# Kernel optimization log

Hardware: AMD Instinct MI355X
Metric: run time of the kernel (lower is better)

The kernel has to match this reference:

```python
import jax, jax.numpy as jnp
import numpy as np

NUM_TRAIN_PTS = 128
KNN = 32
KNN_CLEAN = 4
SIGMA = 0.01
FEAT_DIM = 128
B, N, M = 2, 40000, 40000


def knn_gather(query, pts, k):
    """Brute-force KNN. query [B,Q,3], pts [B,P,3] -> neighbors [B,Q,k,3]."""
    # squared euclidean distances [B,Q,P]
    d2 = (jnp.sum(query * query, -1, keepdims=True)
          - 2.0 * jnp.einsum('bqd,bpd->bqp', query, pts)
          + jnp.sum(pts * pts, -1)[:, None, :])
    _, idx = jax.lax.top_k(-d2, k)                # [B,Q,k]
    nn = jax.vmap(lambda p, i: p[i])(pts, idx)    # gather -> [B,Q,k,3]
    return nn


def setup_inputs() -> dict:
    key = jax.random.key(0)
    k0, k1, k2, k3, k4, k5 = jax.random.split(key, 6)
    noisy_pc = jax.random.uniform(k0, (B, N, 3), dtype=jnp.float32)
    clean_pc = jax.random.uniform(k1, (B, M, 3), dtype=jnp.float32)
    sampled_idx = jax.random.randint(k2, (NUM_TRAIN_PTS,), 0, N)
    Wf = jax.random.normal(k3, (3, FEAT_DIM), dtype=jnp.float32) * 0.1
    Wx = jax.random.normal(k4, (3, 3), dtype=jnp.float32) * 0.1
    Wc = jax.random.normal(k5, (FEAT_DIM, 3), dtype=jnp.float32) * 0.1
    return {'noisy_pc': noisy_pc, 'clean_pc': clean_pc, 'sampled_idx': sampled_idx,
            'Wf': Wf, 'Wx': Wx, 'Wc': Wc}


def reference(noisy_pc, clean_pc, sampled_idx, Wf, Wx, Wc):
    P, K, Kc = NUM_TRAIN_PTS, KNN, KNN_CLEAN
    # per-point feature extraction (stand-in for FeatureExtraction), then sample
    noisy_feat = jnp.einsum('bnd,df->bnf', noisy_pc, Wf)[:, sampled_idx, :]  # [B,P,F]
    q = noisy_pc[:, sampled_idx, :]                                          # [B,P,3]
    # first KNN: neighbors of sampled points within the noisy cloud
    f = knn_gather(q, noisy_pc, K)                                           # [B,P,K,3]
    # score network (stand-in): local offsets + conditioning feature
    estim_score = (jnp.einsum('bpkd,de->bpke', f - q[:, :, None, :], Wx)
                   + jnp.einsum('bpf,fe->bpe', noisy_feat, Wc)[:, :, None, :])  # [B,P,K,3]
    # second KNN: each neighbor point vs the clean cloud (clean shared per batch,
    # avoiding the torch .repeat of clean_pc per training point)
    knn_clean = knn_gather(f.reshape(f.shape[0], P * K, 3), clean_pc, Kc)
    knn_clean = knn_clean.reshape(f.shape[0], P, K, Kc, 3)                   # [B,P,K,Kc,3]
    ground_score = -jnp.mean(f[:, :, :, None, :] - knn_clean, axis=3)        # [B,P,K,3]
    loss = 0.5 * jnp.mean(jnp.sum((estim_score - ground_score) ** 2 * (1.0 / SIGMA), axis=-1))
    return loss
```

## Files before the change

### kernel.cpp

```cpp
#include <hip/hip_runtime.h>
#include <hip/hip_bf16.h>

#define N_PTS   40000
#define N_B     2
#define N_P     128
#define N_K     32
#define N_KC    4
#define N_FEAT  128
#define NQ2     (N_B * N_P * N_K)
#define BIGF    3.0e38f

#define K1SUB   8
#define K1RANGE (N_PTS / K1SUB)
#define QCAP1   512
#define LBUF1   320

#define QCAP    96

#define TAU2    4.0e-3f
#define TAU1    1.6e-2f

#define NG      15
#define NCELL   (NG * NG * NG)
#define GB_BLK  20
#define GB_PER  (N_PTS / GB_BLK)

#define NLOSSB  2048

__device__ int    g_sidx[N_P];
__device__ int    g_fidx[NQ2];
__device__ int    g_q1cnt[256];
__device__ unsigned long long g_q1list[256 * QCAP1];
__device__ int    g_bincnt[N_B * NCELL];
__device__ int    g_binstart[N_B * (NCELL + 1)];
__device__ int    g_cursor[N_B * NCELL];
__device__ float4 g_cpts[N_B * N_PTS];
__device__ int    g_cpidx[N_B * N_PTS];
__device__ float  g_lploss[NLOSSB];
__device__ float  g_M3[9];
__device__ float  g_WxS[9];

__device__ __forceinline__ int clampi(int v, int lo, int hi) { return v < lo ? lo : (v > hi ? hi : v); }

__device__ __forceinline__ unsigned long long packkey(float d, int idx)
{
    unsigned int u = __float_as_uint(d);
    u ^= (u >> 31) ? 0xFFFFFFFFu : 0x80000000u;
    return ((unsigned long long)u << 32) | (unsigned int)idx;
}

__device__ __forceinline__ int cell_of(float x, float y, float z)
{
    const int cx = clampi((int)(x * NG), 0, NG - 1);
    const int cy = clampi((int)(y * NG), 0, NG - 1);
    const int cz = clampi((int)(z * NG), 0, NG - 1);
    return cx + NG * (cy + NG * cz);
}

__global__ __launch_bounds__(256) void setup_kernel(
    const float* __restrict__ clean,
    const void*  __restrict__ sidx_raw,
    const float* __restrict__ Wf,
    const float* __restrict__ Wx,
    const float* __restrict__ Wc)
{
    __shared__ int hist[NCELL];
    __shared__ int flags[4];
    const int blk = blockIdx.x;
    const int tid = threadIdx.x;

    if (blk < N_B * GB_BLK) {
        const int bb = blk / GB_BLK;
        const int sb = blk % GB_BLK;
        const float* cb = clean + bb * (N_PTS * 3);

        for (int i = tid; i < NCELL; i += 256) hist[i] = 0;
        __syncthreads();

        const int j0 = sb * GB_PER;
        for (int j = j0 + tid; j < j0 + GB_PER; j += 256) {
            const float x = cb[j * 3 + 0], y = cb[j * 3 + 1], z = cb[j * 3 + 2];
            atomicAdd(&hist[cell_of(x, y, z)], 1);
        }
        __syncthreads();

        for (int i = tid; i < NCELL; i += 256) {
            const int v = hist[i];
            if (v) atomicAdd(&g_bincnt[bb * NCELL + i], v);
        }
    } else {
        if (tid < 9) {
            const int d = tid / 3, e = tid % 3;
            float acc = 0.0f;
            for (int f0 = 0; f0 < N_FEAT; ++f0)
                acc += Wf[d * N_FEAT + f0] * Wc[f0 * 3 + e];
            g_M3[tid]  = acc;
            g_WxS[tid] = Wx[tid];
        }
        if (tid == 0) { flags[0] = 1; flags[1] = 1; flags[2] = 1; flags[3] = 1; }
        __syncthreads();
        const int*       p32 = (const int*)sidx_raw;
        const long long* p64 = (const long long*)sidx_raw;
        const float*     pf  = (const float*)sidx_raw;
        if (tid < 128) {
            const int       v32 = p32[tid];
            const long long v64 = p64[tid];
            const float     vf  = pf[tid];
            if (!(v32 >= 0 && v32 < N_PTS)) atomicAnd(&flags[0], 0);
            if ((tid & 1) && v32 != 0)      atomicAnd(&flags[1], 0);
            if (!(v64 >= 0 && v64 < N_PTS)) atomicAnd(&flags[2], 0);
            if (!(vf >= 0.0f && vf < (float)N_PTS && vf == floorf(vf))) atomicAnd(&flags[3], 0);
        }
        __syncthreads();
        if (tid < 128) {
            int si;
            if (flags[0] && !(flags[1] && flags[2])) si = p32[tid];
            else if (flags[2])                       si = (int)p64[tid];
            else if (flags[3])                       si = (int)(pf[tid] + 0.5f);
            else                                     si = 0;
            g_sidx[tid] = clampi(si, 0, N_PTS - 1);
        }
    }
}

__global__ __launch_bounds__(256) void scan_knn1_kernel(
    const float* __restrict__ noisy)
{
    __shared__ unsigned long long buf[LBUF1];
    __shared__ int lcnt;
    __shared__ int base_s;
    __shared__ int wsum[4], woff[4];
    const int blk = blockIdx.x;
    const int tid = threadIdx.x;

    if (blk < N_B) {
        const int bb   = blk;
        const int lane = tid & 63, wv = tid >> 6;

        int lvals[14];
        int lsum = 0;
#pragma unroll
        for (int t = 0; t < 14; ++t) {
            const int idx = tid * 14 + t;
            lvals[t] = (idx < NCELL) ? g_bincnt[bb * NCELL + idx] : 0;
            lsum += lvals[t];
        }
        int v = lsum;
#pragma unroll
        for (int off = 1; off < 64; off <<= 1) {
            const int n = __shfl_up(v, off);
            if (lane >= off) v += n;
        }
        if (lane == 63) wsum[wv] = v;
        __syncthreads();
        if (tid == 0) { int r = 0; for (int w = 0; w < 4; ++w) { woff[w] = r; r += wsum[w]; } }
        __syncthreads();

        int run = woff[wv] + (v - lsum);
#pragma unroll
        for (int t = 0; t < 14; ++t) {
            const int idx = tid * 14 + t;
            if (idx < NCELL) {
                g_binstart[bb * (NCELL + 1) + idx] = run;
                g_cursor[bb * NCELL + idx] = run;
                g_bincnt[bb * NCELL + idx] = 0;
                run += lvals[t];
            }
        }
        if (tid == 0) g_binstart[bb * (NCELL + 1) + NCELL] = N_PTS;
    } else {
        const int idx = blk - N_B;
        const int qb  = idx & 255;
        const int sub = idx >> 8;
        const int b   = qb >> 7;
        const int p   = qb & 127;
        const float* nb = noisy + b * (N_PTS * 3);

        if (tid == 0) lcnt = 0;
        const int si = g_sidx[p];
        const float qx = nb[si * 3 + 0];
        const float qy = nb[si * 3 + 1];
        const float qz = nb[si * 3 + 2];
        __syncthreads();

        const int jbeg = sub * K1RANGE;
        const float4* p4 = (const float4*)(nb + jbeg * 3);
        const int nq = K1RANGE / 4;
        for (int q = tid; q < nq; q += 256) {
            const float4 a = p4[q * 3 + 0];
            const float4 c = p4[q * 3 + 1];
            const float4 d = p4[q * 3 + 2];
            const int j = jbeg + q * 4;
            {
                const float dx = qx - a.x, dy = qy - a.y, dz = qz - a.z;
                const float d2 = fmaf(dz, dz, fmaf(dy, dy, dx * dx));
                if (d2 < TAU1) {
                    const int s1 = atomicAdd(&lcnt, 1);
                    if (s1 < LBUF1)
                        buf[s1] = ((unsigned long long)__float_as_uint(d2) << 32) | (unsigned int)(j + 0);
                }
            }
            {
                const float dx = qx - a.w, dy = qy - c.x, dz = qz - c.y;
                const float d2 = fmaf(dz, dz, fmaf(dy, dy, dx * dx));
                if (d2 < TAU1) {
                    const int s1 = atomicAdd(&lcnt, 1);
                    if (s1 < LBUF1)
                        buf[s1] = ((unsigned long long)__float_as_uint(d2) << 32) | (unsigned int)(j + 1);
                }
            }
            {
                const float dx = qx - c.z, dy = qy - c.w, dz = qz - d.x;
                const float d2 = fmaf(dz, dz, fmaf(dy, dy, dx * dx));
                if (d2 < TAU1) {
                    const int s1 = atomicAdd(&lcnt, 1);
                    if (s1 < LBUF1)
                        buf[s1] = ((unsigned long long)__float_as_uint(d2) << 32) | (unsigned int)(j + 2);
                }
            }
            {
                const float dx = qx - d.y, dy = qy - d.z, dz = qz - d.w;
                const float d2 = fmaf(dz, dz, fmaf(dy, dy, dx * dx));
                if (d2 < TAU1) {
                    const int s1 = atomicAdd(&lcnt, 1);
                    if (s1 < LBUF1)
                        buf[s1] = ((unsigned long long)__float_as_uint(d2) << 32) | (unsigned int)(j + 3);
                }
            }
        }
        __syncthreads();

        const int cnt = lcnt;
        if (tid == 0) {
            const int add = (cnt <= LBUF1) ? cnt : (QCAP1 + 1000);
            base_s = atomicAdd(&g_q1cnt[qb], add);
        }
        __syncthreads();

        const int base = base_s;
        const int n = (cnt < LBUF1) ? cnt : LBUF1;
        for (int i = tid; i < n; i += 256) {
            const int o = base + i;
            if (o < QCAP1) g_q1list[qb * QCAP1 + o] = buf[i];
        }
    }
}

__global__ __launch_bounds__(256) void merge_scatter_kernel(
    const float* __restrict__ noisy,
    const float* __restrict__ clean)
{
    __shared__ unsigned long long keys[2048];
    const int blk = blockIdx.x;
    const int tid = threadIdx.x;

    if (blk >= 256) {
        const int idx = blk - 256;
        const int bb  = idx / GB_BLK;
        const int sb  = idx % GB_BLK;
        const float* cb = clean + bb * (N_PTS * 3);

        const int j0 = sb * GB_PER;
        for (int j = j0 + tid; j < j0 + GB_PER; j += 256) {
            const float x = cb[j * 3 + 0], y = cb[j * 3 + 1], z = cb[j * 3 + 2];
            const int c = cell_of(x, y, z);
            const int pos = atomicAdd(&g_cursor[bb * NCELL + c], 1);
            const float pp = fmaf(z, z, fmaf(y, y, x * x));
            g_cpts[bb * N_PTS + pos]  = make_float4(x, y, z, pp);
            g_cpidx[bb * N_PTS + pos] = j;
        }
        return;
    }

    const int qb  = blk;
    const int cnt = g_q1cnt[qb];

    if (cnt >= 32 && cnt <= QCAP1) {
        for (int i = tid; i < QCAP1; i += 256)
            keys[i] = (i < cnt) ? g_q1list[qb * QCAP1 + i] : ~0ULL;
        __syncthreads();
        for (int k = 2; k <= QCAP1; k <<= 1) {
            for (int jj = k >> 1; jj > 0; jj >>= 1) {
                const int idx = tid;
                const int i = ((idx & ~(jj - 1)) << 1) | (idx & (jj - 1));
                const int partner = i | jj;
                const bool asc = ((i & k) == 0);
                const unsigned long long a = keys[i];
                const unsigned long long c = keys[partner];
                if ((a > c) == asc) { keys[i] = c; keys[partner] = a; }
                __syncthreads();
            }
        }
    } else {
        const int b = qb >> 7;
        const float* nb = noisy + b * (N_PTS * 3);
        const int si = g_sidx[qb & 127];
        const float qx = nb[si * 3 + 0];
        const float qy = nb[si * 3 + 1];
        const float qz = nb[si * 3 + 2];

        float bd[8]; int bi[8];
#pragma unroll
        for (int i = 0; i < 8; ++i) { bd[i] = BIGF; bi[i] = 0x7fffffff; }
        for (int j = tid; j < N_PTS; j += 256) {
            const float dx = qx - nb[j * 3 + 0];
            const float dy = qy - nb[j * 3 + 1];
            const float dz = qz - nb[j * 3 + 2];
            const float d2 = fmaf(dz, dz, fmaf(dy, dy, dx * dx));
            if (d2 < bd[7]) {
                bd[7] = d2; bi[7] = j;
#pragma unroll
                for (int t = 7; t > 0; --t) {
                    if (bd[t] < bd[t - 1]) {
                        float td = bd[t]; bd[t] = bd[t - 1]; bd[t - 1] = td;
                        int   ti = bi[t]; bi[t] = bi[t - 1]; bi[t - 1] = ti;
                    }
                }
            }
        }
#pragma unroll
        for (int t = 0; t < 8; ++t)
            keys[tid * 8 + t] = ((unsigned long long)__float_as_uint(bd[t]) << 32)
                              | (unsigned int)bi[t];
        __syncthreads();
        for (int k = 2; k <= 2048; k <<= 1) {
            for (int jj = k >> 1; jj > 0; jj >>= 1) {
#pragma unroll
                for (int base = 0; base < 2048; base += 256) {
                    const int i = base + tid;
                    const int partner = i ^ jj;
                    if (partner > i) {
                        const bool asc = ((i & k) == 0);
                        const unsigned long long a = keys[i];
                        const unsigned long long c = keys[partner];
                        if ((a > c) == asc) { keys[i] = c; keys[partner] = a; }
                    }
                }
                __syncthreads();
            }
        }
    }

    if (tid < 32) {
        const int idx = (int)(keys[tid] & 0xFFFFFFFFull);
        g_fidx[qb * 32 + tid] = clampi(idx, 0, N_PTS - 1);
    }
    if (tid == 0) g_q1cnt[qb] = 0;
}

__global__ __launch_bounds__(256) void knn2_loss_kernel(
    const float* __restrict__ noisy,
    const float* __restrict__ clean)
{
    __shared__ float2 buf[4][QCAP];
    __shared__ int    bcnt[4];
    __shared__ float  red[4];
    const int tid  = threadIdx.x;
    const int wv   = tid >> 6;
    const int lane = tid & 63;
    const int g    = blockIdx.x * 4 + wv;
    const int b    = g >> 12;
    const int p    = (g >> 5) & 127;
    const float* nb = noisy + b * (N_PTS * 3);
    const float* cb = clean + b * (N_PTS * 3);

    if (lane == 0) bcnt[wv] = 0;

    const int fid = clampi(g_fidx[g], 0, N_PTS - 1);
    const float fx = nb[fid * 3 + 0];
    const float fy = nb[fid * 3 + 1];
    const float fz = nb[fid * 3 + 2];
    const float fm2x = -2.0f * fx, fm2y = -2.0f * fy, fm2z = -2.0f * fz;
    const float ff = fmaf(fz, fz, fmaf(fy, fy, fx * fx));
    const float taup = TAU2 - ff;

    const int cfx = clampi((int)(fx * NG), 0, NG - 1);
    const int cfy = clampi((int)(fy * NG), 0, NG - 1);
    const int cfz = clampi((int)(fz * NG), 0, NG - 1);
    const int bso = b * (NCELL + 1);
    const int bpo = b * N_PTS;

    int s = 0, e = 0;
    if (lane < 9) {
        const int cy = cfy + (lane % 3) - 1;
        const int cz = cfz + (lane / 3) - 1;
        if (cy >= 0 && cy < NG && cz >= 0 && cz < NG) {
            const int cxlo = (cfx > 0) ? cfx - 1 : 0;
            const int cxhi = (cfx < NG - 1) ? cfx + 1 : NG - 1;
            const int rowb = NG * (cy + NG * cz);
            s = g_binstart[bso + cxlo + rowb];
            e = g_binstart[bso + cxhi + rowb + 1];
        }
    }
    const int len = e - s;
    int incl = len;
#pragma unroll
    for (int off = 1; off < 16; off <<= 1) {
        const int nsh = __shfl_up(incl, off);
        if (lane >= off) incl += nsh;
    }
    const int T = __shfl(incl, 8);
    const int pfx = incl - len;

    int rp[9], rs[9];
#pragma unroll
    for (int i = 0; i < 9; ++i) {
        rp[i] = __shfl(pfx, i);
        rs[i] = __shfl(s, i);
    }

    for (int t = lane; t < T; t += 64) {
        int base = rs[0], pref = rp[0];
#pragma unroll
        for (int i = 1; i < 9; ++i) {
            const bool gsel = (t >= rp[i]);
            base = gsel ? rs[i] : base;
            pref = gsel ? rp[i] : pref;
        }
        const int k = base + (t - pref);
        const float4 pt = g_cpts[bpo + k];
        const float d2 = fmaf(fm2x, pt.x, fmaf(fm2y, pt.y, fmaf(fm2z, pt.z, pt.w)));
        if (d2 < taup) {
            const int slot = atomicAdd(&bcnt[wv], 1);
            if (slot < QCAP)
                buf[wv][slot] = make_float2(d2, __int_as_float(g_cpidx[bpo + k]));
        }
    }
    __syncthreads();

    const int cnt = bcnt[wv];
    int nn[4];

    if (cnt >= 4 && cnt <= QCAP) {
        unsigned long long e0 = ~0ULL, e1 = ~0ULL;
        if (lane < cnt) {
            const float2 a = buf[wv][lane];
            e0 = packkey(a.x, __float_as_int(a.y));
        }
        if (lane + 64 < cnt) {
            const float2 a = buf[wv][lane + 64];
            e1 = packkey(a.x, __float_as_int(a.y));
        }
        if (e1 < e0) { unsigned long long t = e0; e0 = e1; e1 = t; }

        int c = 0;
#pragma unroll
        for (int r = 0; r < 4; ++r) {
            const unsigned long long h = (c == 0) ? e0 : ((c == 1) ? e1 : ~0ULL);
            unsigned long long m = h;
#pragma unroll
            for (int off = 32; off; off >>= 1) {
                const unsigned long long o = __shfl_xor(m, off);
                if (o < m) m = o;
            }
            if (h == m) c++;
            nn[r] = (int)(m & 0xFFFFFFFFull);
        }
    } else {
        float bd[4]; int bi[4];
#pragma unroll
        for (int t = 0; t < 4; ++t) { bd[t] = BIGF; bi[t] = 0x7fffffff; }
        for (int j = lane; j < N_PTS; j += 64) {
            const float dx = fx - cb[j * 3 + 0];
            const float dy = fy - cb[j * 3 + 1];
            const float dz = fz - cb[j * 3 + 2];
            const float d2 = fmaf(dz, dz, fmaf(dy, dy, dx * dx));
            if (d2 < bd[3]) {
                bd[3] = d2; bi[3] = j;
#pragma unroll
                for (int t = 3; t > 0; --t) {
                    if (bd[t] < bd[t - 1]) {
                        float td = bd[t]; bd[t] = bd[t - 1]; bd[t - 1] = td;
                        int   ti = bi[t]; bi[t] = bi[t - 1]; bi[t - 1] = ti;
                    }
                }
            }
        }
        int cur = 0;
        for (int r = 0; r < 4; ++r) {
            float v  = (cur < 4) ? bd[cur] : BIGF;
            int   vi = (cur < 4) ? bi[cur] : 0x7fffffff;
            int   who = lane;
#pragma unroll
            for (int off = 32; off; off >>= 1) {
                const float v2  = __shfl_down(v, off);
                const int   vi2 = __shfl_down(vi, off);
                const int   w2  = __shfl_down(who, off);
                if (v2 < v || (v2 == v && vi2 < vi)) { v = v2; vi = vi2; who = w2; }
            }
            const int bvi = __shfl(vi, 0);
            const int bwh = __shfl(who, 0);
            nn[r] = bvi;
            if (lane == bwh) cur++;
        }
    }

    float t2 = 0.0f;
    if (lane == 0) {
        const int si = g_sidx[p];
        const float qx = nb[si * 3 + 0], qy = nb[si * 3 + 1], qz = nb[si * 3 + 2];
        const int n0 = clampi(nn[0], 0, N_PTS - 1), n1 = clampi(nn[1], 0, N_PTS - 1);
        const int n2 = clampi(nn[2], 0, N_PTS - 1), n3 = clampi(nn[3], 0, N_PTS - 1);
        const float mx = 0.25f * (cb[n0*3+0] + cb[n1*3+0] + cb[n2*3+0] + cb[n3*3+0]);
        const float my = 0.25f * (cb[n0*3+1] + cb[n1*3+1] + cb[n2*3+1] + cb[n3*3+1]);
        const float mz = 0.25f * (cb[n0*3+2] + cb[n1*3+2] + cb[n2*3+2] + cb[n3*3+2]);

        const float gx = mx - fx, gy = my - fy, gz = mz - fz;
        const float rx = fx - qx, ry = fy - qy, rz = fz - qz;
        const float ex = rx * g_WxS[0] + ry * g_WxS[3] + rz * g_WxS[6] + qx * g_M3[0] + qy * g_M3[3] + qz * g_M3[6];
        const float ey = rx * g_WxS[1] + ry * g_WxS[4] + rz * g_WxS[7] + qx * g_M3[1] + qy * g_M3[4] + qz * g_M3[7];
        const float ez = rx * g_WxS[2] + ry * g_WxS[5] + rz * g_WxS[8] + qx * g_M3[2] + qy * g_M3[5] + qz * g_M3[8];
        const float dx = ex - gx, dy = ey - gy, dz = ez - gz;
        t2 = dx * dx + dy * dy + dz * dz;
    }

    if (lane == 0) red[wv] = t2;
    __syncthreads();
    if (tid == 0) g_lploss[blockIdx.x] = (red[0] + red[1]) + (red[2] + red[3]);
}

__global__ __launch_bounds__(256) void final_kernel(float* __restrict__ out)
{
    __shared__ float red[4];
    const int tid = threadIdx.x;
    float v = 0.0f;
    for (int i = tid; i < NLOSSB; i += 256) v += g_lploss[i];
#pragma unroll
    for (int off = 32; off; off >>= 1) v += __shfl_down(v, off);
    if ((tid & 63) == 0) red[tid >> 6] = v;
    __syncthreads();
    if (tid == 0) out[0] = ((red[0] + red[1]) + (red[2] + red[3])) * (50.0f / 8192.0f);
}

extern "C" void kernel_launch(void* const* d_in, const int* in_sizes, int n_in,
                              void* d_out, int out_size, void* d_ws, size_t ws_size,
                              hipStream_t stream)
{
    (void)d_ws; (void)ws_size; (void)in_sizes; (void)n_in; (void)out_size;

    const float* noisy = (const float*)d_in[0];
    const float* clean = (const float*)d_in[1];
    const float* Wf    = (const float*)d_in[3];
    const float* Wx    = (const float*)d_in[4];
    const float* Wc    = (const float*)d_in[5];

    setup_kernel<<<N_B * GB_BLK + 1, 256, 0, stream>>>(clean, d_in[2], Wf, Wx, Wc);
    scan_knn1_kernel<<<N_B + 256 * K1SUB, 256, 0, stream>>>(noisy);
    merge_scatter_kernel<<<256 + N_B * GB_BLK, 256, 0, stream>>>(noisy, clean);
    knn2_loss_kernel<<<NLOSSB, 256, 0, stream>>>(noisy, clean);
    final_kernel<<<1, 256, 0, stream>>>((float*)d_out);
}
```

Before: 103.7 us.

## Fuse setup into scan_knn1 kernel and build clean-grid histogram per batch block

Merges the setup kernel into the KNN1 scan kernel, which removes one launch and the dependency between them. Each KNN1 block now decodes the sampled index itself instead of reading g_sidx. One block per batch builds the full clean-cloud cell histogram in shared memory with vectorized loads and then scans it directly, dropping the global bincnt atomics and the separate reset. The cost is that those two histogram blocks each process 40000 points serially and may become the critical path, and every scan block redoes the index-format detection.

```diff
diff --git a/kernel.cpp b/kernel.cpp
--- a/kernel.cpp
+++ b/kernel.cpp
@@ -22,6 +22,7 @@
 
 #define NG      15
 #define NCELL   (NG * NG * NG)
+
 #define GB_BLK  20
 #define GB_PER  (N_PTS / GB_BLK)
 
@@ -31,7 +32,6 @@
 __device__ int    g_fidx[NQ2];
 __device__ int    g_q1cnt[256];
 __device__ unsigned long long g_q1list[256 * QCAP1];
-__device__ int    g_bincnt[N_B * NCELL];
 __device__ int    g_binstart[N_B * (NCELL + 1)];
 __device__ int    g_cursor[N_B * NCELL];
 __device__ float4 g_cpts[N_B * N_PTS];
@@ -57,7 +57,8 @@
     return cx + NG * (cy + NG * cz);
 }
 
-__global__ __launch_bounds__(256) void setup_kernel(
+__global__ __launch_bounds__(256) void scan_knn1_kernel(
+    const float* __restrict__ noisy,
     const float* __restrict__ clean,
     const void*  __restrict__ sidx_raw,
     const float* __restrict__ Wf,
@@ -65,43 +66,79 @@
     const float* __restrict__ Wc)
 {
     __shared__ int hist[NCELL];
+    __shared__ unsigned long long buf[LBUF1];
+    __shared__ int lcnt;
+    __shared__ int base_s;
+    __shared__ int wsum[4], woff[4];
     __shared__ int flags[4];
     const int blk = blockIdx.x;
     const int tid = threadIdx.x;
 
-    if (blk < N_B * GB_BLK) {
-        const int bb = blk / GB_BLK;
-        const int sb = blk % GB_BLK;
+    const int*       p32 = (const int*)sidx_raw;
+    const long long* p64 = (const long long*)sidx_raw;
+    const float*     pf  = (const float*)sidx_raw;
+
+    if (blk < N_B) {
+        const int bb = blk;
         const float* cb = clean + bb * (N_PTS * 3);
 
         for (int i = tid; i < NCELL; i += 256) hist[i] = 0;
         __syncthreads();
 
-        const int j0 = sb * GB_PER;
-        for (int j = j0 + tid; j < j0 + GB_PER; j += 256) {
-            const float x = cb[j * 3 + 0], y = cb[j * 3 + 1], z = cb[j * 3 + 2];
-            atomicAdd(&hist[cell_of(x, y, z)], 1);
-        }
-        __syncthreads();
-
-        for (int i = tid; i < NCELL; i += 256) {
-            const int v = hist[i];
-            if (v) atomicAdd(&g_bincnt[bb * NCELL + i], v);
-        }
-    } else {
-        if (tid < 9) {
-            const int d = tid / 3, e = tid % 3;
-            float acc = 0.0f;
-            for (int f0 = 0; f0 < N_FEAT; ++f0)
-                acc += Wf[d * N_FEAT + f0] * Wc[f0 * 3 + e];
-            g_M3[tid]  = acc;
-            g_WxS[tid] = Wx[tid];
-        }
-        if (tid == 0) { flags[0] = 1; flags[1] = 1; flags[2] = 1; flags[3] = 1; }
-        __syncthreads();
-        const int*       p32 = (const int*)sidx_raw;
-        const long long* p64 = (const long long*)sidx_raw;
-        const float*     pf  = (const float*)sidx_raw;
+        const float4* c4 = (const float4*)cb;
+        const int nq = N_PTS / 4;
+        for (int q = tid; q < nq; q += 256) {
+            const float4 a = c4[q * 3 + 0];
+            const float4 c = c4[q * 3 + 1];
+            const float4 d = c4[q * 3 + 2];
+            atomicAdd(&hist[cell_of(a.x, a.y, a.z)], 1);
+            atomicAdd(&hist[cell_of(a.w, c.x, c.y)], 1);
+            atomicAdd(&hist[cell_of(c.z, c.w, d.x)], 1);
+            atomicAdd(&hist[cell_of(d.y, d.z, d.w)], 1);
+        }
+        __syncthreads();
+
+        const int lane = tid & 63, wv = tid >> 6;
+        int lvals[14];
+        int lsum = 0;
+#pragma unroll
+        for (int t = 0; t < 14; ++t) {
+            const int idx = tid * 14 + t;
+            lvals[t] = (idx < NCELL) ? hist[idx] : 0;
+            lsum += lvals[t];
+        }
+        int v = lsum;
+#pragma unroll
+        for (int off = 1; off < 64; off <<= 1) {
+            const int n = __shfl_up(v, off);
+            if (lane >= off) v += n;
+        }
+        if (lane == 63) wsum[wv] = v;
+        __syncthreads();
+        if (tid == 0) { int r = 0; for (int w = 0; w < 4; ++w) { woff[w] = r; r += wsum[w]; } }
+        __syncthreads();
+
+        int run = woff[wv] + (v - lsum);
+#pragma unroll
+        for (int t = 0; t < 14; ++t) {
+            const int idx = tid * 14 + t;
+            if (idx < NCELL) {
+                g_binstart[bb * (NCELL + 1) + idx] = run;
+                g_cursor[bb * NCELL + idx] = run;
+                run += lvals[t];
+            }
+        }
+        if (tid == 0) g_binstart[bb * (NCELL + 1) + NCELL] = N_PTS;
+    } else if (blk < N_B + 256 * K1SUB) {
+        const int idx = blk - N_B;
+        const int qb  = idx & 255;
+        const int sub = idx >> 8;
+        const int b   = qb >> 7;
+        const int p   = qb & 127;
+        const float* nb = noisy + b * (N_PTS * 3);
+
+        if (tid == 0) { lcnt = 0; flags[0] = 1; flags[1] = 1; flags[2] = 1; flags[3] = 1; }
+        __syncthreads();
         if (tid < 128) {
             const int       v32 = p32[tid];
             const long long v64 = p64[tid];
@@ -112,76 +149,15 @@
             if (!(vf >= 0.0f && vf < (float)N_PTS && vf == floorf(vf))) atomicAnd(&flags[3], 0);
         }
         __syncthreads();
-        if (tid < 128) {
-            int si;
-            if (flags[0] && !(flags[1] && flags[2])) si = p32[tid];
-            else if (flags[2])                       si = (int)p64[tid];
-            else if (flags[3])                       si = (int)(pf[tid] + 0.5f);
-            else                                     si = 0;
-            g_sidx[tid] = clampi(si, 0, N_PTS - 1);
-        }
-    }
-}
-
-__global__ __launch_bounds__(256) void scan_knn1_kernel(
-    const float* __restrict__ noisy)
-{
-    __shared__ unsigned long long buf[LBUF1];
-    __shared__ int lcnt;
-    __shared__ int base_s;
-    __shared__ int wsum[4], woff[4];
-    const int blk = blockIdx.x;
-    const int tid = threadIdx.x;
-
-    if (blk < N_B) {
-        const int bb   = blk;
-        const int lane = tid & 63, wv = tid >> 6;
-
-        int lvals[14];
-        int lsum = 0;
-#pragma unroll
-        for (int t = 0; t < 14; ++t) {
-            const int idx = tid * 14 + t;
-            lvals[t] = (idx < NCELL) ? g_bincnt[bb * NCELL + idx] : 0;
-            lsum += lvals[t];
-        }
-        int v = lsum;
-#pragma unroll
-        for (int off = 1; off < 64; off <<= 1) {
-            const int n = __shfl_up(v, off);
-            if (lane >= off) v += n;
-        }
-        if (lane == 63) wsum[wv] = v;
-        __syncthreads();
-        if (tid == 0) { int r = 0; for (int w = 0; w < 4; ++w) { woff[w] = r; r += wsum[w]; } }
-        __syncthreads();
-
-        int run = woff[wv] + (v - lsum);
-#pragma unroll
-        for (int t = 0; t < 14; ++t) {
-            const int idx = tid * 14 + t;
-            if (idx < NCELL) {
-                g_binstart[bb * (NCELL + 1) + idx] = run;
-                g_cursor[bb * NCELL + idx] = run;
-                g_bincnt[bb * NCELL + idx] = 0;
-                run += lvals[t];
-            }
-        }
-        if (tid == 0) g_binstart[bb * (NCELL + 1) + NCELL] = N_PTS;
-    } else {
-        const int idx = blk - N_B;
-        const int qb  = idx & 255;
-        const int sub = idx >> 8;
-        const int b   = qb >> 7;
-        const int p   = qb & 127;
-        const float* nb = noisy + b * (N_PTS * 3);
-
-        if (tid == 0) lcnt = 0;
-        const int si = g_sidx[p];
+        int si;
+        if (flags[0] && !(flags[1] && flags[2])) si = p32[p];
+        else if (flags[2])                       si = (int)p64[p];
+        else if (flags[3])                       si = (int)(pf[p] + 0.5f);
+        else                                     si = 0;
+        si = clampi(si, 0, N_PTS - 1);
         const float qx = nb[si * 3 + 0];
         const float qy = nb[si * 3 + 1];
         const float qz = nb[si * 3 + 2];
-        __syncthreads();
 
         const int jbeg = sub * K1RANGE;
         const float4* p4 = (const float4*)(nb + jbeg * 3);
@@ -243,6 +219,35 @@
             const int o = base + i;
             if (o < QCAP1) g_q1list[qb * QCAP1 + o] = buf[i];
         }
+    } else {
+        if (tid < 9) {
+            const int d = tid / 3, e = tid % 3;
+            float acc = 0.0f;
+            for (int f0 = 0; f0 < N_FEAT; ++f0)
+                acc += Wf[d * N_FEAT + f0] * Wc[f0 * 3 + e];
+            g_M3[tid]  = acc;
+            g_WxS[tid] = Wx[tid];
+        }
+        if (tid == 0) { flags[0] = 1; flags[1] = 1; flags[2] = 1; flags[3] = 1; }
+        __syncthreads();
+        if (tid < 128) {
+            const int       v32 = p32[tid];
+            const long long v64 = p64[tid];
+            const float     vf  = pf[tid];
+            if (!(v32 >= 0 && v32 < N_PTS)) atomicAnd(&flags[0], 0);
+            if ((tid & 1) && v32 != 0)      atomicAnd(&flags[1], 0);
+            if (!(v64 >= 0 && v64 < N_PTS)) atomicAnd(&flags[2], 0);
+            if (!(vf >= 0.0f && vf < (float)N_PTS && vf == floorf(vf))) atomicAnd(&flags[3], 0);
+        }
+        __syncthreads();
+        if (tid < 128) {
+            int si;
+            if (flags[0] && !(flags[1] && flags[2])) si = p32[tid];
+            else if (flags[2])                       si = (int)p64[tid];
+            else if (flags[3])                       si = (int)(pf[tid] + 0.5f);
+            else                                     si = 0;
+            g_sidx[tid] = clampi(si, 0, N_PTS - 1);
+        }
     }
 }
 
@@ -544,8 +549,7 @@
     const float* Wx    = (const float*)d_in[4];
     const float* Wc    = (const float*)d_in[5];
 
-    setup_kernel<<<N_B * GB_BLK + 1, 256, 0, stream>>>(clean, d_in[2], Wf, Wx, Wc);
-    scan_knn1_kernel<<<N_B + 256 * K1SUB, 256, 0, stream>>>(noisy);
+    scan_knn1_kernel<<<N_B + 256 * K1SUB + 1, 256, 0, stream>>>(noisy, clean, d_in[2], Wf, Wx, Wc);
     merge_scatter_kernel<<<256 + N_B * GB_BLK, 256, 0, stream>>>(noisy, clean);
     knn2_loss_kernel<<<NLOSSB, 256, 0, stream>>>(noisy, clean);
     final_kernel<<<1, 256, 0, stream>>>((float*)d_out);
```

Measured after the change: 112.6 us. +8.5%, slower.
